# Performance work log

Measured on AMD Instinct MI355X. Metric: run time of the kernel, lower is better.

The kernel has to match this reference:

```python
import jax, jax.numpy as jnp
import numpy as np

N = 50000      # nodes
E = 160000     # edges
NFEAT = 1024
NHID = 512
NCLASS = 64


def _unif(k, shape, fan):
    s = 1.0 / np.sqrt(fan)
    return jax.random.uniform(k, shape, jnp.float32, -s, s)


def setup_inputs() -> dict:
    key = jax.random.key(0)
    ks = jax.random.split(key, 16)
    x = jax.random.normal(ks[0], (N, NFEAT), jnp.float32)
    adj_row = jax.random.randint(ks[1], (E,), 0, N, jnp.int32)
    adj_col = jax.random.randint(ks[2], (E,), 0, N, jnp.int32)
    adj_val = jax.random.uniform(ks[3], (E,), jnp.float32)
    # gc1: nfeat -> nhid (stdv = 1/sqrt(out_features))
    W1 = _unif(ks[4], (NFEAT, NHID), NHID)
    b1 = _unif(ks[5], (NHID,), NHID)
    # residual projection for gc1 (nn.Linear nfeat->nhid)
    p1W = _unif(ks[6], (NFEAT, NHID), NFEAT)
    p1b = _unif(ks[7], (NHID,), NFEAT)
    # gc3: nhid -> nhid (shared across 4 applications)
    W3 = _unif(ks[8], (NHID, NHID), NHID)
    b3 = _unif(ks[9], (NHID,), NHID)
    # gc2: nhid -> nclass
    W2 = _unif(ks[10], (NHID, NCLASS), NCLASS)
    b2 = _unif(ks[11], (NCLASS,), NCLASS)
    # residual projection for gc2 (nn.Linear nhid->nclass)
    p2W = _unif(ks[12], (NHID, NCLASS), NHID)
    p2b = _unif(ks[13], (NCLASS,), NHID)
    return {"x": x, "adj_row": adj_row, "adj_col": adj_col, "adj_val": adj_val,
            "W1": W1, "b1": b1, "p1W": p1W, "p1b": p1b,
            "W3": W3, "b3": b3, "W2": W2, "b2": b2, "p2W": p2W, "p2b": p2b}


def _spmm(row, col, val, support):
    # out[i] = sum_e val[e] * support[col[e]] for row[e] == i   (adj @ support)
    return jax.ops.segment_sum(val[:, None] * support[col], row, num_segments=N)


def reference(x, adj_row, adj_col, adj_val, W1, b1, p1W, p1b, W3, b3, W2, b2, p2W, p2b):
    def gc_proj(inp, W, b, pW, pb):
        # shapes differ -> projected residual
        out = _spmm(adj_row, adj_col, adj_val, inp @ W) + b
        return jax.nn.relu(out + inp @ pW + pb)

    def gc_res(inp, W, b):
        # same shape -> identity residual
        out = _spmm(adj_row, adj_col, adj_val, inp @ W) + b
        return jax.nn.relu(out + inp)

    h = jax.nn.relu(gc_proj(x, W1, b1, p1W, p1b))       # [N, NHID]
    for _ in range(4):                                   # gc3 shared weights x4
        h = jax.nn.relu(gc_res(h, W3, b3))
    h = gc_proj(h, W2, b2, p2W, p2b)                     # [N, NCLASS]
    return jax.nn.log_softmax(h, axis=1)
```

## Files before the change

kernel.cpp:

```cpp
#include <hip/hip_runtime.h>

typedef __attribute__((ext_vector_type(8))) short bf16x8;
typedef __attribute__((ext_vector_type(8))) unsigned short ushort8;
typedef __attribute__((ext_vector_type(4))) float f32x4;

#define NNODES 50000
#define NEDGES 160000
#define MP     50176
#define NB_SCAN 196

__device__ __forceinline__ float bf2f(unsigned short u) {
  return __uint_as_float(((unsigned int)u) << 16);
}
__device__ __forceinline__ unsigned short f2bf(float f) {
  unsigned int u = __float_as_uint(f);
  u += 0x7fffu + ((u >> 16) & 1u);
  return (unsigned short)(u >> 16);
}
__device__ __forceinline__ void gld16(const void* g, void* l) {
  __builtin_amdgcn_global_load_lds((__attribute__((address_space(1))) void*)g,
                                   (__attribute__((address_space(3))) void*)l, 16, 0, 0);
}

__global__ void k_hist(const int* __restrict__ row, int* __restrict__ cnt, int n) {
  int i = blockIdx.x * 256 + threadIdx.x;
  if (i < n) atomicAdd(&cnt[row[i]], 1);
}

__global__ void k_block_reduce(const int* __restrict__ cnt, int* __restrict__ bsum, int n) {
  __shared__ int sd[256];
  int i = blockIdx.x * 256 + threadIdx.x;
  sd[threadIdx.x] = (i < n) ? cnt[i] : 0;
  __syncthreads();
  for (int o = 128; o > 0; o >>= 1) {
    if (threadIdx.x < o) sd[threadIdx.x] += sd[threadIdx.x + o];
    __syncthreads();
  }
  if (threadIdx.x == 0) bsum[blockIdx.x] = sd[0];
}

__global__ void k_scan_bsum(const int* __restrict__ bsum, int* __restrict__ boff, int nb,
                            int* __restrict__ rowptr, int n, int E) {
  __shared__ int sd[256];
  int v = (threadIdx.x < nb) ? bsum[threadIdx.x] : 0;
  sd[threadIdx.x] = v;
  __syncthreads();
  for (int o = 1; o < 256; o <<= 1) {
    int t = (threadIdx.x >= o) ? sd[threadIdx.x - o] : 0;
    __syncthreads();
    sd[threadIdx.x] += t;
    __syncthreads();
  }
  if (threadIdx.x < nb) boff[threadIdx.x] = sd[threadIdx.x] - v;
  if (threadIdx.x == 0) rowptr[n] = E;
}

__global__ void k_block_scan(const int* __restrict__ cnt, const int* __restrict__ boff,
                             int* __restrict__ rowptr, int* __restrict__ cursor, int n) {
  __shared__ int sd[256];
  int i = blockIdx.x * 256 + threadIdx.x;
  int v = (i < n) ? cnt[i] : 0;
  sd[threadIdx.x] = v;
  __syncthreads();
  for (int o = 1; o < 256; o <<= 1) {
    int t = (threadIdx.x >= o) ? sd[threadIdx.x - o] : 0;
    __syncthreads();
    sd[threadIdx.x] += t;
    __syncthreads();
  }
  if (i < n) {
    int r = boff[blockIdx.x] + sd[threadIdx.x] - v;
    rowptr[i] = r;
    cursor[i] = r;
  }
}

__global__ void k_scatter(const int* __restrict__ row, const int* __restrict__ col,
                          const float* __restrict__ val, int* __restrict__ cursor,
                          int* __restrict__ scol, float* __restrict__ sval, int n) {
  int e = blockIdx.x * 256 + threadIdx.x;
  if (e < n) {
    int p = atomicAdd(&cursor[row[e]], 1);
    scol[p] = col[e];
    sval[p] = val[e];
  }
}

__global__ void k_cast_x(const float* __restrict__ x, unsigned short* __restrict__ xb, int nRealRows) {
  size_t idx = ((size_t)blockIdx.x * 256 + threadIdx.x) * 8;
  if (idx >= (size_t)MP * 1024) return;
  int row = (int)(idx >> 10);
  ushort8 o;
  if (row < nRealRows) {
    float4 a = *(const float4*)(x + idx);
    float4 b = *(const float4*)(x + idx + 4);
    o[0] = f2bf(a.x); o[1] = f2bf(a.y); o[2] = f2bf(a.z); o[3] = f2bf(a.w);
    o[4] = f2bf(b.x); o[5] = f2bf(b.y); o[6] = f2bf(b.z); o[7] = f2bf(b.w);
  } else {
    o = (ushort8){0,0,0,0,0,0,0,0};
  }
  *(ushort8*)(xb + idx) = o;
}

__global__ void k_pack_all(const float* __restrict__ W1, const float* __restrict__ p1W,
                           const float* __restrict__ W3, const float* __restrict__ W2,
                           const float* __restrict__ p2W,
                           const float* __restrict__ b1, const float* __restrict__ p1b,
                           const float* __restrict__ b2, const float* __restrict__ p2b,
                           unsigned short* __restrict__ B1t, unsigned short* __restrict__ W3t,
                           unsigned short* __restrict__ B2t,
                           float* __restrict__ bias1, float* __restrict__ bias2) {
  int z = blockIdx.z;
  int tx = threadIdx.x, ty = threadIdx.y;
  if (z == 5) {
    if (blockIdx.x || blockIdx.y) return;
    int t = ty * 32 + tx;
    bias1[t] = b1[t] + p1b[t];
    bias1[t + 256] = b1[t + 256] + p1b[t + 256];
    if (t < 64) bias2[t] = b2[t] + p2b[t];
    return;
  }
  const float* src; unsigned short* dst; int K, srcW, nc, dstOff;
  if (z == 0)      { src = W1;  dst = B1t; K = 1024; srcW = 512; nc = 512; dstOff = 0; }
  else if (z == 1) { src = p1W; dst = B1t; K = 1024; srcW = 512; nc = 512; dstOff = 512; }
  else if (z == 2) { src = W3;  dst = W3t; K = 512;  srcW = 512; nc = 512; dstOff = 0; }
  else if (z == 3) { src = W2;  dst = B2t; K = 512;  srcW = 64;  nc = 64;  dstOff = 0; }
  else             { src = p2W; dst = B2t; K = 512;  srcW = 64;  nc = 64;  dstOff = 64; }
  int k0 = blockIdx.x * 32, n0 = blockIdx.y * 32;
  if (k0 >= K || n0 >= nc) return;
  __shared__ float tile[32][33];
  for (int i = ty; i < 32; i += 8)
    tile[i][tx] = src[(size_t)(k0 + i) * srcW + (n0 + tx)];
  __syncthreads();
  for (int i = ty; i < 32; i += 8)
    dst[(size_t)(dstOff + n0 + i) * K + (k0 + tx)] = f2bf(tile[tx][i]);
}

__global__ __launch_bounds__(512, 4) void k_gemm128x256(
    const unsigned short* __restrict__ A, const unsigned short* __restrict__ Bt,
    unsigned short* __restrict__ C, int M, int N, int K) {
  extern __shared__ char smem[];
  const int NT = N >> 8;
  const int nwg = gridDim.x;
  const int q = nwg >> 3, r = nwg & 7;
  const int xcd = blockIdx.x & 7, local = blockIdx.x >> 3;
  const int swz = (xcd < r ? xcd * (q + 1) : r * (q + 1) + (xcd - r) * q) + local;
  const int mt = swz / NT, nt = swz % NT;

  const int tid = threadIdx.x;
  const int w = tid >> 6, lane = tid & 63;
  const int wr = w >> 2, wc = w & 3;

  const int srow = tid >> 2;
  const int schunk = (tid & 3) ^ ((tid >> 3) & 3);
  const unsigned short* gA = A + (size_t)(mt * 128 + srow) * K + schunk * 8;
  const unsigned short* gB = Bt + (size_t)(nt * 256 + srow) * K + schunk * 8;
  const size_t rs128 = (size_t)128 * K;
  const int wb = w << 10;

  const int l15 = lane & 15;
  const int cpos = ((lane >> 4) ^ ((l15 >> 1) & 3)) << 4;
  const int aOff = (wr * 64 + l15) * 64 + cpos;
  const int bOff = 8192 + (wc * 64 + l15) * 64 + cpos;

  f32x4 acc[4][4] = {};
  const int T = K >> 5;

  auto STAGE = [&](int t) {
    char* db = smem + (t % 3) * 24576 + wb;
    const unsigned short* a = gA + t * 32;
    const unsigned short* b = gB + t * 32;
    gld16(a, db);
    gld16(b, db + 8192);
    gld16(b + rs128, db + 16384);
  };

  STAGE(0); STAGE(1);

  for (int t = 0; t < T; ++t) {
    if (t < T - 1) asm volatile("s_waitcnt vmcnt(3)" ::: "memory");
    else           asm volatile("s_waitcnt vmcnt(0)" ::: "memory");
    __builtin_amdgcn_s_barrier();
    __builtin_amdgcn_sched_barrier(0);
    if (t + 2 < T) STAGE(t + 2);
    const int bb = (t % 3) * 24576;
    bf16x8 af[4];
#pragma unroll
    for (int m = 0; m < 4; ++m) af[m] = *(const bf16x8*)(smem + bb + aOff + m * 1024);
    __builtin_amdgcn_s_setprio(1);
#pragma unroll
    for (int n = 0; n < 4; ++n) {
      bf16x8 bfr = *(const bf16x8*)(smem + bb + bOff + n * 1024);
#pragma unroll
      for (int m = 0; m < 4; ++m)
        acc[m][n] = __builtin_amdgcn_mfma_f32_16x16x32_bf16(af[m], bfr, acc[m][n], 0, 0, 0);
    }
    __builtin_amdgcn_s_setprio(0);
  }

  const int r0 = mt * 128 + wr * 64 + (lane >> 4) * 4;
  const int c0e = nt * 256 + wc * 64 + l15;
#pragma unroll
  for (int m = 0; m < 4; ++m)
#pragma unroll
    for (int n = 0; n < 4; ++n)
#pragma unroll
      for (int j = 0; j < 4; ++j)
        C[(size_t)(r0 + m * 16 + j) * N + (c0e + n * 16)] = f2bf(acc[m][n][j]);
}

__global__ __launch_bounds__(256, 4) void k_gemm128(
    const unsigned short* __restrict__ A, const unsigned short* __restrict__ Bt,
    unsigned short* __restrict__ C, int M, int N, int K) {
  extern __shared__ char smem[];
  const int NT = N >> 7;
  const int nwg = gridDim.x;
  const int q = nwg >> 3, r = nwg & 7;
  const int xcd = blockIdx.x & 7, local = blockIdx.x >> 3;
  const int swz = (xcd < r ? xcd * (q + 1) : r * (q + 1) + (xcd - r) * q) + local;
  const int mt = swz / NT, nt = swz % NT;

  const int tid = threadIdx.x;
  const int w = tid >> 6, lane = tid & 63;
  const int wr = w >> 1, wc = w & 1;

  const int srow = tid >> 2;
  const int schunk = (tid & 3) ^ ((srow >> 1) & 3);
  const unsigned short* gA = A + (size_t)(mt * 128 + srow) * K + schunk * 8;
  const unsigned short* gB = Bt + (size_t)(nt * 128 + srow) * K + schunk * 8;
  const size_t rs64 = (size_t)64 * K;
  const int wb = w << 10;

  const int l15 = lane & 15;
  const int cpos = ((lane >> 4) ^ ((l15 >> 1) & 3)) << 4;
  const int aOff = (wr * 64 + l15) * 64 + cpos;
  const int bOff = 8192 + (wc * 64 + l15) * 64 + cpos;

  f32x4 acc[4][4] = {};
  const int T = K >> 5;

  auto STAGE = [&](int t) {
    char* db = smem + (t % 3) * 16384 + wb;
    const unsigned short* a = gA + t * 32;
    const unsigned short* b = gB + t * 32;
    gld16(a, db);
    gld16(a + rs64, db + 4096);
    gld16(b, db + 8192);
    gld16(b + rs64, db + 12288);
  };

  STAGE(0); STAGE(1);

  for (int t = 0; t < T; ++t) {
    if (t < T - 1) asm volatile("s_waitcnt vmcnt(4)" ::: "memory");
    else           asm volatile("s_waitcnt vmcnt(0)" ::: "memory");
    __builtin_amdgcn_s_barrier();
    __builtin_amdgcn_sched_barrier(0);
    if (t + 2 < T) STAGE(t + 2);
    const int bb = (t % 3) * 16384;
    bf16x8 af[4];
#pragma unroll
    for (int m = 0; m < 4; ++m) af[m] = *(const bf16x8*)(smem + bb + aOff + m * 1024);
    __builtin_amdgcn_s_setprio(1);
#pragma unroll
    for (int n = 0; n < 4; ++n) {
      bf16x8 bfr = *(const bf16x8*)(smem + bb + bOff + n * 1024);
#pragma unroll
      for (int m = 0; m < 4; ++m)
        acc[m][n] = __builtin_amdgcn_mfma_f32_16x16x32_bf16(af[m], bfr, acc[m][n], 0, 0, 0);
    }
    __builtin_amdgcn_s_setprio(0);
  }

  const int r0 = mt * 128 + wr * 64 + (lane >> 4) * 4;
  const int c0e = nt * 128 + wc * 64 + l15;
#pragma unroll
  for (int m = 0; m < 4; ++m)
#pragma unroll
    for (int n = 0; n < 4; ++n)
#pragma unroll
      for (int j = 0; j < 4; ++j)
        C[(size_t)(r0 + m * 16 + j) * N + (c0e + n * 16)] = f2bf(acc[m][n][j]);
}

__global__ __launch_bounds__(256) void k_spmm_ep512(
    const int* __restrict__ rowptr, const int* __restrict__ scol, const float* __restrict__ sval,
    const unsigned short* __restrict__ s, int sStride,
    const unsigned short* __restrict__ res, int resStride,
    const float* __restrict__ bias,
    unsigned short* __restrict__ o, int oStride, int nReal, int nTot) {
  int gw = (blockIdx.x * 256 + threadIdx.x) >> 6;
  int lane = threadIdx.x & 63;
  if (gw >= nTot) return;
  unsigned short* op = o + (size_t)gw * oStride + lane * 8;
  if (gw >= nReal) {
    *(ushort8*)op = (ushort8){0,0,0,0,0,0,0,0};
    return;
  }
  float acc[8] = {0.f,0.f,0.f,0.f,0.f,0.f,0.f,0.f};
  int e0 = rowptr[gw], e1 = rowptr[gw + 1];
  int e = e0;
  for (; e + 4 <= e1; e += 4) {
    int c0 = scol[e], c1 = scol[e + 1], c2 = scol[e + 2], c3 = scol[e + 3];
    float v0 = sval[e], v1 = sval[e + 1], v2 = sval[e + 2], v3 = sval[e + 3];
    ushort8 s0 = *(const ushort8*)(s + (size_t)c0 * sStride + lane * 8);
    ushort8 s1 = *(const ushort8*)(s + (size_t)c1 * sStride + lane * 8);
    ushort8 s2 = *(const ushort8*)(s + (size_t)c2 * sStride + lane * 8);
    ushort8 s3 = *(const ushort8*)(s + (size_t)c3 * sStride + lane * 8);
#pragma unroll
    for (int k = 0; k < 8; ++k)
      acc[k] += v0 * bf2f(s0[k]) + v1 * bf2f(s1[k]) + v2 * bf2f(s2[k]) + v3 * bf2f(s3[k]);
  }
  if (e + 2 <= e1) {
    int c0 = scol[e], c1 = scol[e + 1];
    float v0 = sval[e], v1 = sval[e + 1];
    ushort8 s0 = *(const ushort8*)(s + (size_t)c0 * sStride + lane * 8);
    ushort8 s1 = *(const ushort8*)(s + (size_t)c1 * sStride + lane * 8);
#pragma unroll
    for (int k = 0; k < 8; ++k) acc[k] += v0 * bf2f(s0[k]) + v1 * bf2f(s1[k]);
    e += 2;
  }
  if (e < e1) {
    int c = scol[e];
    float v = sval[e];
    ushort8 sv = *(const ushort8*)(s + (size_t)c * sStride + lane * 8);
#pragma unroll
    for (int k = 0; k < 8; ++k) acc[k] += v * bf2f(sv[k]);
  }
  ushort8 rv = *(const ushort8*)(res + (size_t)gw * resStride + lane * 8);
  ushort8 ov;
#pragma unroll
  for (int k = 0; k < 8; ++k) {
    float tt = acc[k] + bias[lane * 8 + k] + bf2f(rv[k]);
    ov[k] = f2bf(fmaxf(tt, 0.f));
  }
  *(ushort8*)op = ov;
}

__global__ __launch_bounds__(256) void k_spmm_lsm(
    const int* __restrict__ rowptr, const int* __restrict__ scol, const float* __restrict__ sval,
    const unsigned short* __restrict__ g2, const float* __restrict__ bias2,
    float* __restrict__ out, int n) {
  int gw = (blockIdx.x * 256 + threadIdx.x) >> 6;
  int lane = threadIdx.x & 63;
  if (gw >= n) return;
  int e0 = rowptr[gw], e1 = rowptr[gw + 1];
  float acc = 0.f;
  int e = e0;
  for (; e + 2 <= e1; e += 2) {
    int c0 = scol[e], c1 = scol[e + 1];
    float v0 = sval[e], v1 = sval[e + 1];
    float a0 = bf2f(g2[(size_t)c0 * 128 + lane]);
    float a1 = bf2f(g2[(size_t)c1 * 128 + lane]);
    acc += v0 * a0 + v1 * a1;
  }
  if (e < e1) acc += sval[e] * bf2f(g2[(size_t)scol[e] * 128 + lane]);
  float t = acc + bias2[lane] + bf2f(g2[(size_t)gw * 128 + 64 + lane]);
  float v = fmaxf(t, 0.f);
  float m = v;
#pragma unroll
  for (int o = 32; o > 0; o >>= 1) m = fmaxf(m, __shfl_xor(m, o));
  float ex = __expf(v - m);
  float ss = ex;
#pragma unroll
  for (int o = 32; o > 0; o >>= 1) ss += __shfl_xor(ss, o);
  out[(size_t)gw * 64 + lane] = v - m - __logf(ss);
}

extern "C" void kernel_launch(void* const* d_in, const int* in_sizes, int n_in,
                              void* d_out, int out_size, void* d_ws, size_t ws_size,
                              hipStream_t stream) {
  const float* x    = (const float*)d_in[0];
  const int*   arow = (const int*)d_in[1];
  const int*   acol = (const int*)d_in[2];
  const float* aval = (const float*)d_in[3];
  const float* W1   = (const float*)d_in[4];
  const float* b1   = (const float*)d_in[5];
  const float* p1W  = (const float*)d_in[6];
  const float* p1b  = (const float*)d_in[7];
  const float* W3   = (const float*)d_in[8];
  const float* b3   = (const float*)d_in[9];
  const float* W2   = (const float*)d_in[10];
  const float* b2   = (const float*)d_in[11];
  const float* p2W  = (const float*)d_in[12];
  const float* p2b  = (const float*)d_in[13];
  float* out = (float*)d_out;

  char* wsp = (char*)d_ws;
  size_t off = 0;
  auto take = [&](size_t bytes) -> char* {
    char* p = wsp + off;
    off = (off + bytes + 255) & ~(size_t)255;
    return p;
  };
  unsigned short* xb  = (unsigned short*)take((size_t)MP * 1024 * 2);
  unsigned short* g1  = (unsigned short*)take((size_t)MP * 1024 * 2);
  unsigned short* B1t = (unsigned short*)take((size_t)1024 * 1024 * 2);
  unsigned short* W3t = (unsigned short*)take((size_t)512 * 512 * 2);
  unsigned short* B2t = (unsigned short*)take((size_t)128 * 512 * 2);
  float* bias1 = (float*)take(512 * 4);
  float* bias2 = (float*)take(64 * 4);
  int*   cnt    = (int*)take((size_t)NNODES * 4);
  int*   rowptr = (int*)take((size_t)(NNODES + 1) * 4);
  int*   bsum   = (int*)take(256 * 4);
  int*   boff   = (int*)take(256 * 4);
  int*   scol   = (int*)take((size_t)NEDGES * 4);
  float* sval   = (float*)take((size_t)NEDGES * 4);
  unsigned short* h  = xb;
  unsigned short* s  = g1;
  unsigned short* g2 = g1;

  hipMemsetAsync(cnt, 0, (size_t)NNODES * 4, stream);
  k_hist<<<(NEDGES + 255) / 256, 256, 0, stream>>>(arow, cnt, NEDGES);
  k_block_reduce<<<NB_SCAN, 256, 0, stream>>>(cnt, bsum, NNODES);
  k_scan_bsum<<<1, 256, 0, stream>>>(bsum, boff, NB_SCAN, rowptr, NNODES, NEDGES);
  k_block_scan<<<NB_SCAN, 256, 0, stream>>>(cnt, boff, rowptr, cnt, NNODES);
  k_scatter<<<(NEDGES + 255) / 256, 256, 0, stream>>>(arow, acol, aval, cnt, scol, sval, NEDGES);

  k_cast_x<<<(int)(((size_t)MP * 1024 / 8 + 255) / 256), 256, 0, stream>>>(x, xb, NNODES);
  k_pack_all<<<dim3(32, 16, 6), dim3(32, 8), 0, stream>>>(W1, p1W, W3, W2, p2W,
                                                          b1, p1b, b2, p2b,
                                                          B1t, W3t, B2t, bias1, bias2);

  k_gemm128x256<<<392 * 4, 512, 73728, stream>>>(xb, B1t, g1, MP, 1024, 1024);
  k_spmm_ep512<<<MP / 4, 256, 0, stream>>>(rowptr, scol, sval, g1, 1024, g1 + 512, 1024,
                                           bias1, h, 512, NNODES, MP);
  for (int i = 0; i < 4; ++i) {
    k_gemm128<<<392 * 4, 256, 49152, stream>>>(h, W3t, s, MP, 512, 512);
    k_spmm_ep512<<<MP / 4, 256, 0, stream>>>(rowptr, scol, sval, s, 512, h, 512,
                                             b3, h, 512, NNODES, MP);
  }
  k_gemm128<<<392, 256, 49152, stream>>>(h, B2t, g2, MP, 128, 512);
  k_spmm_lsm<<<(NNODES + 3) / 4, 256, 0, stream>>>(rowptr, scol, sval, g2, bias2, out, NNODES);
}
```

Measured before the change: 583.6 us.

## Fuse fp32-to-bf16 cast of x into first GEMM A-tile loading

Removes the standalone cast kernel and has the first GEMM load fp32 rows of x directly into registers, convert them to bf16, and write swizzled tiles into LDS. B tiles still use async global-to-LDS loads, and the loop is unrolled by two to double-buffer the A registers. This avoids writing and re-reading a bf16 copy of x, but the GEMM now reads fp32 A data (twice the bytes per tile, repeated across N tiles) and does conversion work in the inner loop. h gets its own buffer since xb is gone.

```diff
diff --git a/kernel.cpp b/kernel.cpp
--- a/kernel.cpp
+++ b/kernel.cpp
@@ -84,22 +84,6 @@
     scol[p] = col[e];
     sval[p] = val[e];
   }
-}
-
-__global__ void k_cast_x(const float* __restrict__ x, unsigned short* __restrict__ xb, int nRealRows) {
-  size_t idx = ((size_t)blockIdx.x * 256 + threadIdx.x) * 8;
-  if (idx >= (size_t)MP * 1024) return;
-  int row = (int)(idx >> 10);
-  ushort8 o;
-  if (row < nRealRows) {
-    float4 a = *(const float4*)(x + idx);
-    float4 b = *(const float4*)(x + idx + 4);
-    o[0] = f2bf(a.x); o[1] = f2bf(a.y); o[2] = f2bf(a.z); o[3] = f2bf(a.w);
-    o[4] = f2bf(b.x); o[5] = f2bf(b.y); o[6] = f2bf(b.z); o[7] = f2bf(b.w);
-  } else {
-    o = (ushort8){0,0,0,0,0,0,0,0};
-  }
-  *(ushort8*)(xb + idx) = o;
 }
 
 __global__ void k_pack_all(const float* __restrict__ W1, const float* __restrict__ p1W,
@@ -136,9 +120,9 @@
     dst[(size_t)(dstOff + n0 + i) * K + (k0 + tx)] = f2bf(tile[tx][i]);
 }
 
-__global__ __launch_bounds__(512, 4) void k_gemm128x256(
-    const unsigned short* __restrict__ A, const unsigned short* __restrict__ Bt,
-    unsigned short* __restrict__ C, int M, int N, int K) {
+__global__ __launch_bounds__(512, 4) void k_gemm1f(
+    const float* __restrict__ X, const unsigned short* __restrict__ Bt,
+    unsigned short* __restrict__ C, int M, int N, int K, int nReal) {
   extern __shared__ char smem[];
   const int NT = N >> 8;
   const int nwg = gridDim.x;
@@ -151,10 +135,20 @@
   const int w = tid >> 6, lane = tid & 63;
   const int wr = w >> 2, wc = w & 3;
 
-  const int srow = tid >> 2;
-  const int schunk = (tid & 3) ^ ((tid >> 3) & 3);
-  const unsigned short* gA = A + (size_t)(mt * 128 + srow) * K + schunk * 8;
-  const unsigned short* gB = Bt + (size_t)(nt * 256 + srow) * K + schunk * 8;
+  const int arow = tid >> 3;
+  const int k4 = tid & 7;
+  const int ar0 = mt * 128 + arow;
+  const int ar1 = ar0 + 64;
+  const bool ok0 = ar0 < nReal, ok1 = ar1 < nReal;
+  const float* gx0 = X + (size_t)ar0 * K + k4 * 4;
+  const float* gx1 = X + (size_t)ar1 * K + k4 * 4;
+  const int arow1 = arow + 64;
+  const int ac0 = arow * 64 + (((k4 >> 1) ^ ((arow >> 1) & 3)) << 4) + (k4 & 1) * 8;
+  const int ac1 = arow1 * 64 + (((k4 >> 1) ^ ((arow1 >> 1) & 3)) << 4) + (k4 & 1) * 8;
+
+  const int brow = tid >> 2;
+  const int bchunk = (tid & 3) ^ ((brow >> 1) & 3);
+  const unsigned short* gB = Bt + (size_t)(nt * 256 + brow) * K + bchunk * 8;
   const size_t rs128 = (size_t)128 * K;
   const int wb = w << 10;
 
@@ -165,25 +159,26 @@
 
   f32x4 acc[4][4] = {};
   const int T = K >> 5;
-
-  auto STAGE = [&](int t) {
+  float4 aE0, aE1, aO0, aO1;
+  const float4 fz = {0.f, 0.f, 0.f, 0.f};
+
+  auto STAGE_B = [&](int t) {
     char* db = smem + (t % 3) * 24576 + wb;
-    const unsigned short* a = gA + t * 32;
     const unsigned short* b = gB + t * 32;
-    gld16(a, db);
     gld16(b, db + 8192);
     gld16(b + rs128, db + 16384);
   };
-
-  STAGE(0); STAGE(1);
-
-  for (int t = 0; t < T; ++t) {
-    if (t < T - 1) asm volatile("s_waitcnt vmcnt(3)" ::: "memory");
-    else           asm volatile("s_waitcnt vmcnt(0)" ::: "memory");
-    __builtin_amdgcn_s_barrier();
-    __builtin_amdgcn_sched_barrier(0);
-    if (t + 2 < T) STAGE(t + 2);
-    const int bb = (t % 3) * 24576;
+  auto WRITE_A = [&](int buf, const float4& q0, const float4& q1) {
+    char* base = smem + buf * 24576;
+    uint2 u0, u1;
+    u0.x = (unsigned)f2bf(q0.x) | ((unsigned)f2bf(q0.y) << 16);
+    u0.y = (unsigned)f2bf(q0.z) | ((unsigned)f2bf(q0.w) << 16);
+    u1.x = (unsigned)f2bf(q1.x) | ((unsigned)f2bf(q1.y) << 16);
+    u1.y = (unsigned)f2bf(q1.z) | ((unsigned)f2bf(q1.w) << 16);
+    *(uint2*)(base + ac0) = u0;
+    *(uint2*)(base + ac1) = u1;
+  };
+  auto COMPUTE = [&](int bb) {
     bf16x8 af[4];
 #pragma unroll
     for (int m = 0; m < 4; ++m) af[m] = *(const bf16x8*)(smem + bb + aOff + m * 1024);
@@ -196,6 +191,40 @@
         acc[m][n] = __builtin_amdgcn_mfma_f32_16x16x32_bf16(af[m], bfr, acc[m][n], 0, 0, 0);
     }
     __builtin_amdgcn_s_setprio(0);
+  };
+
+  aE0 = ok0 ? *(const float4*)(gx0) : fz;
+  aE1 = ok1 ? *(const float4*)(gx1) : fz;
+  STAGE_B(0);
+  aO0 = ok0 ? *(const float4*)(gx0 + 32) : fz;
+  aO1 = ok1 ? *(const float4*)(gx1 + 32) : fz;
+  STAGE_B(1);
+
+  for (int t = 0; t < T; t += 2) {
+    asm volatile("s_waitcnt vmcnt(4)" ::: "memory");
+    WRITE_A(t % 3, aE0, aE1);
+    asm volatile("s_waitcnt lgkmcnt(0)" ::: "memory");
+    __builtin_amdgcn_s_barrier();
+    __builtin_amdgcn_sched_barrier(0);
+    if (t + 2 < T) {
+      aE0 = ok0 ? *(const float4*)(gx0 + (t + 2) * 32) : fz;
+      aE1 = ok1 ? *(const float4*)(gx1 + (t + 2) * 32) : fz;
+      STAGE_B(t + 2);
+    }
+    COMPUTE((t % 3) * 24576);
+    const int u = t + 1;
+    if (u < T - 1) asm volatile("s_waitcnt vmcnt(4)" ::: "memory");
+    else           asm volatile("s_waitcnt vmcnt(0)" ::: "memory");
+    WRITE_A(u % 3, aO0, aO1);
+    asm volatile("s_waitcnt lgkmcnt(0)" ::: "memory");
+    __builtin_amdgcn_s_barrier();
+    __builtin_amdgcn_sched_barrier(0);
+    if (u + 2 < T) {
+      aO0 = ok0 ? *(const float4*)(gx0 + (u + 2) * 32) : fz;
+      aO1 = ok1 ? *(const float4*)(gx1 + (u + 2) * 32) : fz;
+      STAGE_B(u + 2);
+    }
+    COMPUTE((u % 3) * 24576);
   }
 
   const int r0 = mt * 128 + wr * 64 + (lane >> 4) * 4;
@@ -393,8 +422,8 @@
     off = (off + bytes + 255) & ~(size_t)255;
     return p;
   };
-  unsigned short* xb  = (unsigned short*)take((size_t)MP * 1024 * 2);
   unsigned short* g1  = (unsigned short*)take((size_t)MP * 1024 * 2);
+  unsigned short* h   = (unsigned short*)take((size_t)MP * 512 * 2);
   unsigned short* B1t = (unsigned short*)take((size_t)1024 * 1024 * 2);
   unsigned short* W3t = (unsigned short*)take((size_t)512 * 512 * 2);
   unsigned short* B2t = (unsigned short*)take((size_t)128 * 512 * 2);
@@ -406,7 +435,6 @@
   int*   boff   = (int*)take(256 * 4);
   int*   scol   = (int*)take((size_t)NEDGES * 4);
   float* sval   = (float*)take((size_t)NEDGES * 4);
-  unsigned short* h  = xb;
   unsigned short* s  = g1;
   unsigned short* g2 = g1;
 
@@ -417,12 +445,11 @@
   k_block_scan<<<NB_SCAN, 256, 0, stream>>>(cnt, boff, rowptr, cnt, NNODES);
   k_scatter<<<(NEDGES + 255) / 256, 256, 0, stream>>>(arow, acol, aval, cnt, scol, sval, NEDGES);
 
-  k_cast_x<<<(int)(((size_t)MP * 1024 / 8 + 255) / 256), 256, 0, stream>>>(x, xb, NNODES);
   k_pack_all<<<dim3(32, 16, 6), dim3(32, 8), 0, stream>>>(W1, p1W, W3, W2, p2W,
                                                           b1, p1b, b2, p2b,
                                                           B1t, W3t, B2t, bias1, bias2);
 
-  k_gemm128x256<<<392 * 4, 512, 73728, stream>>>(xb, B1t, g1, MP, 1024, 1024);
+  k_gemm1f<<<392 * 4, 512, 73728, stream>>>(x, B1t, g1, MP, 1024, 1024, NNODES);
   k_spmm_ep512<<<MP / 4, 256, 0, stream>>>(rowptr, scol, sval, g1, 1024, g1 + 512, 1024,
                                            bias1, h, 512, NNODES, MP);
   for (int i = 0; i < 4; ++i) {
```

Result: slower. 710.9 us (+21.8%).
